# Optimization experiments

Hardware: AMD Instinct MI355X
Metric: run time of the kernel (lower is better)

## Reference

```python
import jax, jax.numpy as jnp
import numpy as np
from jax import lax

# --- COSMO-SAC constants (defaults from the layer) ---
T = 623.15
Q0 = 79.53
R0 = 66.69
C_HB = 85580.0
RGAS = 8.3144598 / 4184.0
SIG_HB = 0.0084
EPS = 3.667
AEFF = 7.5
EO = 0.0002395
ZC = 10.0
X0 = 0.235
X1 = 1.0 - 0.235
N_SIGMA = 51
N_ITERS = 50


def _deltaw():
    s = np.linspace(-0.025, 0.025, N_SIGMA)
    sigma_m = np.tile(s, (N_SIGMA, 1))          # rows of grid values
    sigma_n = sigma_m.T
    sigma_acc = np.tril(sigma_n) + np.triu(sigma_m, 1)
    sigma_don = np.tril(sigma_m) + np.triu(sigma_n, 1)
    fpol = (EPS - 1.0) / (EPS + 0.5)
    alpha = 0.3 * AEFF ** 1.5 / EO
    alpha_prime = fpol * alpha
    dw = (alpha_prime / 2.0 * (sigma_m + sigma_n) ** 2
          + C_HB * np.maximum(0.0, sigma_acc - SIG_HB) * np.minimum(0.0, sigma_don + SIG_HB))
    return jnp.asarray(dw, jnp.float32)

DELTAW = _deltaw()                       # [51,51]
SSS = jnp.exp(-DELTAW / (RGAS * T))      # [51,51]


def get_Gamma(psigma):
    """50-step fixed-point solve. psigma: [B,51] -> Gamma: [B,51]."""
    AA = SSS[None, :, :] * psigma[:, None, :]   # [B,51,51]
    def step(G, _):
        Gnew = 1.0 / jnp.einsum('bmn,bn->bm', AA, G)
        return (Gnew + G) * 0.5, None
    G, _ = lax.scan(step, jnp.ones_like(psigma), None, length=N_ITERS)
    return G


def setup_inputs() -> dict:
    key = jax.random.key(0)
    k1, k2, k3, k4 = jax.random.split(key, 4)
    B = 32768
    return {
        "input_my_sigma": jax.random.uniform(k1, (B, N_SIGMA), dtype=jnp.float32),
        "v_compound": jax.random.uniform(k2, (B,), dtype=jnp.float32),
        "input_vt_sigma": jax.random.uniform(k3, (B, N_SIGMA, 2), dtype=jnp.float32),
        "v_vt": jax.random.uniform(k4, (B,), dtype=jnp.float32),
    }


def reference(input_my_sigma, v_compound, input_vt_sigma, v_vt):
    my = input_my_sigma                 # [B,51]
    vt = input_vt_sigma[:, :, 1]        # [B,51]
    A0 = jnp.sum(my, axis=1)            # [B]
    A1 = jnp.sum(vt, axis=1)            # [B]

    psigma_mix = (X0 * my + X1 * vt) / (X0 * A0[:, None] + X1 * A1[:, None])
    lnGamma_mix = jnp.log(get_Gamma(psigma_mix))       # [B,51]

    # residual part for component i = 0
    psigma = my / A0[:, None]
    lnGammai = jnp.log(get_Gamma(psigma))              # [B,51]
    lng_resid = A0 / AEFF * jnp.sum(psigma * (lnGamma_mix - lnGammai), axis=1)

    # combinatorial part (Staverman-Guggenheim)
    q0 = A0 / Q0
    q1 = A1 / Q0
    r0 = v_compound / R0
    r1 = v_vt / R0
    xq = X0 * q0 + X1 * q1
    xr = X0 * r0 + X1 * r1
    theta = X0 * q0 / xq
    phi = X0 * r0 / xr
    l0 = ZC / 2.0 * (r0 - q0) - (r0 - 1.0)
    l1 = ZC / 2.0 * (r1 - q1) - (r1 - 1.0)
    xl = X0 * l0 + X1 * l1
    lng_comb = (jnp.log(phi / X0) + ZC / 2.0 * q0 * jnp.log(theta / phi)
                + l0 - phi / X0 * xl)

    return (lng_resid + lng_comb)[:, None]             # [B,1]
```

## Files before the change

### kernel.cpp

```cpp
#include <hip/hip_runtime.h>

typedef __bf16 bf16;
typedef __attribute__((ext_vector_type(8))) bf16 bf16x8;
typedef __attribute__((ext_vector_type(4))) float f32x4;

namespace {

constexpr int NITERS = 50;
constexpr int KEXACT = 16;

constexpr double csqrt(double x) {
  double s = x > 1 ? x : 1;
  for (int i = 0; i < 60; ++i) s = 0.5 * (s + x / s);
  return s;
}
constexpr double AP_D =
    ((3.667 - 1.0) / (3.667 + 0.5)) * (0.3 * (7.5 * csqrt(7.5)) / 0.0002395);
constexpr double RGAST_D = (8.3144598 / 4184.0) * 623.15;

__device__ __forceinline__ float sss_val(int i, int j) {
  if (i > 50 || j > 50) return 0.0f;
  const float si = -0.025f + 0.001f * (float)i;
  const float sj = -0.025f + 0.001f * (float)j;
  const float acc = fmaxf(0.0f, fmaxf(si, sj) - 0.0084f);
  const float don = fminf(0.0f, fminf(si, sj) + 0.0084f);
  const float dw = (float)(AP_D * 0.5) * (si + sj) * (si + sj) + 85580.0f * acc * don;
  return expf(-dw * (float)(1.0 / RGAST_D));
}

__device__ __forceinline__ int slot2row(int slot) {
  if (slot < 48) return slot;
  if ((slot & 3) == 0 && slot < 60) return 48 + ((slot - 48) >> 2);
  return 99;
}

__device__ __forceinline__ float fast_log(float x) {
  return __builtin_amdgcn_logf(x) * 0.69314718056f;
}

__device__ __forceinline__ f32x4 mfma(bf16x8 a, bf16x8 b, f32x4 c) {
  return __builtin_amdgcn_mfma_f32_16x16x32_bf16(a, b, c, 0, 0, 0);
}

__device__ __forceinline__ unsigned cvt_pk(float lo, float hi) {
  unsigned r;
  asm("v_cvt_pk_bf16_f32 %0, %1, %2" : "=v"(r) : "v"(lo), "v"(hi));
  return r;
}

union B8 { unsigned u[4]; bf16x8 v; };

}

__global__ __launch_bounds__(256, 4) void cosmo_mfma_r8(
    const float* __restrict__ my_sigma,
    const float* __restrict__ v_comp,
    const float* __restrict__ vt_sigma,
    const float* __restrict__ v_vt,
    float* __restrict__ out,
    int B)
{
  const int lane = threadIdx.x & 63;
  const int wv   = threadIdx.x >> 6;
  const int s    = lane & 15;
  const int g    = lane >> 4;
  const int task = s & 1;
  const int e    = blockIdx.x * 32 + wv * 8 + (s >> 1);
  const bool ein = (e < B);
  const int  ec  = ein ? e : 0;

  float A0, A1;
  float wh[13], Gt[13], rc[13];
  {
    float myv[13], vtv[13];
#pragma unroll
    for (int t = 0; t < 4; ++t)
#pragma unroll
      for (int r = 0; r < 4; ++r) {
        const int li = 4 * t + r;
        if (li >= 13) continue;
        const int n  = slot2row(16 * t + 4 * g + r);
        const bool nv = (n < 51) && ein;
        const int nc = (n < 51) ? n : 50;
        myv[li] = nv ? my_sigma[(size_t)ec * 51 + nc] : 0.0f;
        vtv[li] = nv ? vt_sigma[((size_t)ec * 51 + nc) * 2 + 1] : 0.0f;
      }
    float pA0 = 0.f, pA1 = 0.f;
#pragma unroll
    for (int i = 0; i < 13; ++i) { pA0 += myv[i]; pA1 += vtv[i]; }
    pA0 += __shfl_xor(pA0, 16, 64); pA0 += __shfl_xor(pA0, 32, 64);
    pA1 += __shfl_xor(pA1, 16, 64); pA1 += __shfl_xor(pA1, 32, 64);
    A0 = pA0; A1 = pA1;

    const float den  = task ? (0.235f * pA0 + 0.765f * pA1) : pA0;
    const float rden = __builtin_amdgcn_rcpf(den);
    const float rdh  = 0.5f * rden;
#pragma unroll
    for (int i = 0; i < 13; ++i) {
      const float num = task ? (0.235f * myv[i] + 0.765f * vtv[i]) : myv[i];
      Gt[i] = num * rden;
      wh[i] = num * rdh;
      rc[i] = 1.0f;
    }
  }

  bf16x8 afr[4][2];
#pragma unroll
  for (int tp = 0; tp < 4; ++tp)
#pragma unroll
    for (int kt = 0; kt < 2; ++kt) {
      bf16x8 v;
#pragma unroll
      for (int i = 0; i < 8; ++i) {
        const int kslot = 16 * (2 * kt + (i >> 2)) + 4 * g + (i & 3);
        v[i] = (bf16)sss_val(slot2row(16 * tp + s), slot2row(kslot));
      }
      afr[tp][kt] = v;
    }

  f32x4 pad3;
  pad3[0] = (g == 3) ? 1.0f : 0.0f;
  pad3[1] = pad3[2] = pad3[3] = 1.0f;

  f32x4 acc[4];

  auto matvec = [&]() {
    B8 x0, x1;
    x0.u[0] = cvt_pk(Gt[0],  Gt[1]);
    x0.u[1] = cvt_pk(Gt[2],  Gt[3]);
    x0.u[2] = cvt_pk(Gt[4],  Gt[5]);
    x0.u[3] = cvt_pk(Gt[6],  Gt[7]);
    x1.u[0] = cvt_pk(Gt[8],  Gt[9]);
    x1.u[1] = cvt_pk(Gt[10], Gt[11]);
    x1.u[2] = cvt_pk(Gt[12], 0.0f);
    x1.u[3] = 0;
    const bf16x8 b0 = x0.v, b1 = x1.v;

    const f32x4 z = {};
#pragma unroll
    for (int tp = 0; tp < 3; ++tp) acc[tp] = mfma(afr[tp][0], b0, z);
    acc[3] = mfma(afr[3][0], b0, pad3);
#pragma unroll
    for (int tp = 0; tp < 4; ++tp) acc[tp] = mfma(afr[tp][1], b1, acc[tp]);
  };

  auto upd_rcp = [&]() {
#pragma unroll
    for (int tp = 0; tp < 3; ++tp)
#pragma unroll
      for (int r = 0; r < 4; ++r) {
        const int i = 4 * tp + r;
        const float rcv = __builtin_amdgcn_rcpf(acc[tp][r]);
        rc[i] = rcv;
        Gt[i] = __builtin_fmaf(wh[i], rcv, 0.5f * Gt[i]);
      }
    {
      const float rcv = __builtin_amdgcn_rcpf(acc[3][0]);
      rc[12] = rcv;
      Gt[12] = __builtin_fmaf(wh[12], rcv, 0.5f * Gt[12]);
    }
  };

  auto upd_newton = [&]() {
#pragma unroll
    for (int tp = 0; tp < 3; ++tp)
#pragma unroll
      for (int r = 0; r < 4; ++r) {
        const int i = 4 * tp + r;
        const float nr  = __builtin_fmaf(-acc[tp][r], rc[i], 2.0f);
        const float rcv = rc[i] * nr;
        rc[i] = rcv;
        Gt[i] = __builtin_fmaf(wh[i], rcv, 0.5f * Gt[i]);
      }
    {
      const float nr  = __builtin_fmaf(-acc[3][0], rc[12], 2.0f);
      const float rcv = rc[12] * nr;
      rc[12] = rcv;
      Gt[12] = __builtin_fmaf(wh[12], rcv, 0.5f * Gt[12]);
    }
  };

  matvec();
#pragma unroll
  for (int it = 0; it < KEXACT; ++it) { upd_rcp(); matvec(); }
#pragma unroll
  for (int it = KEXACT; it < NITERS - 1; ++it) { upd_newton(); matvec(); }
  upd_newton();

  const float rA0 = __builtin_amdgcn_rcpf(A0);
  float Sp = 0.f;
#pragma unroll
  for (int t = 0; t < 4; ++t)
#pragma unroll
    for (int r = 0; r < 4; ++r) {
      const int li = 4 * t + r;
      if (li >= 13) continue;
      const int n = slot2row(16 * t + 4 * g + r);
      if (n < 51) {
        const float p  = (ein ? my_sigma[(size_t)ec * 51 + n] : 0.0f) * rA0;
        const float gg = (wh[li] != 0.0f)
                           ? Gt[li] * (0.5f * __builtin_amdgcn_rcpf(wh[li])) : 1.0f;
        Sp += p * __builtin_amdgcn_logf(gg);
      }
    }
  Sp += __shfl_xor(Sp, 16, 64);
  Sp += __shfl_xor(Sp, 32, 64);
  const float St = Sp * 0.69314718056f;
  const float So = __shfl_xor(St, 1, 64);

  if (task == 0 && g == 0 && ein) {
    const float lng_resid = A0 * (1.0f / 7.5f) * (So - St);
    const float v0  = v_comp[e];
    const float v1v = v_vt[e];
    const float q0 = A0 * (1.0f / 79.53f), q1 = A1 * (1.0f / 79.53f);
    const float r0 = v0 * (1.0f / 66.69f), r1 = v1v * (1.0f / 66.69f);
    const float xq = 0.235f * q0 + 0.765f * q1;
    const float xr = 0.235f * r0 + 0.765f * r1;
    const float theta = 0.235f * q0 * __builtin_amdgcn_rcpf(xq);
    const float phi   = 0.235f * r0 * __builtin_amdgcn_rcpf(xr);
    const float l0 = 5.0f * (r0 - q0) - (r0 - 1.0f);
    const float l1 = 5.0f * (r1 - q1) - (r1 - 1.0f);
    const float xl = 0.235f * l0 + 0.765f * l1;
    const float lng_comb = fast_log(phi * (1.0f / 0.235f))
                         + 5.0f * q0 * fast_log(theta * __builtin_amdgcn_rcpf(phi))
                         + l0 - (phi * (1.0f / 0.235f)) * xl;
    out[e] = lng_resid + lng_comb;
  }
}

extern "C" void kernel_launch(void* const* d_in, const int* in_sizes, int n_in,
                              void* d_out, int out_size, void* d_ws, size_t ws_size,
                              hipStream_t stream) {
  const float* my  = (const float*)d_in[0];
  const float* vc  = (const float*)d_in[1];
  const float* vts = (const float*)d_in[2];
  const float* vvt = (const float*)d_in[3];
  float* out = (float*)d_out;
  const int B = in_sizes[1];
  const int grid = (B + 31) / 32;
  cosmo_mfma_r8<<<grid, 256, 0, stream>>>(my, vc, vts, vvt, out, B);
}
```

Baseline: 109.6 us.

## Switch fixed-point matvec to 32x32x16 MFMA with 16 systems per wave

Replaces the 16x16x32 MFMA tiling with 32x32x16 bf16 MFMAs. Each wave now handles 32 right-hand sides (16 elements × 2 tasks) against a 64-row padded SSS matrix, so the compact slot remapping is no longer needed. This doubles the elements per block and halves the grid. The iteration loops are no longer unrolled and the occupancy hint drops to 2, trading more registers per lane for fewer MFMA issues per element. It also pads to 64 rows instead of the tighter 51-row packing, so some of the extra work is wasted.

```diff
diff --git a/kernel.cpp b/kernel.cpp
--- a/kernel.cpp
+++ b/kernel.cpp
@@ -2,7 +2,7 @@
 
 typedef __bf16 bf16;
 typedef __attribute__((ext_vector_type(8))) bf16 bf16x8;
-typedef __attribute__((ext_vector_type(4))) float f32x4;
+typedef __attribute__((ext_vector_type(16))) float f32x16;
 
 namespace {
 
@@ -28,18 +28,12 @@
   return expf(-dw * (float)(1.0 / RGAST_D));
 }
 
-__device__ __forceinline__ int slot2row(int slot) {
-  if (slot < 48) return slot;
-  if ((slot & 3) == 0 && slot < 60) return 48 + ((slot - 48) >> 2);
-  return 99;
-}
-
 __device__ __forceinline__ float fast_log(float x) {
   return __builtin_amdgcn_logf(x) * 0.69314718056f;
 }
 
-__device__ __forceinline__ f32x4 mfma(bf16x8 a, bf16x8 b, f32x4 c) {
-  return __builtin_amdgcn_mfma_f32_16x16x32_bf16(a, b, c, 0, 0, 0);
+__device__ __forceinline__ f32x16 mfma32(bf16x8 a, bf16x8 b, f32x16 c) {
+  return __builtin_amdgcn_mfma_f32_32x32x16_bf16(a, b, c, 0, 0, 0);
 }
 
 __device__ __forceinline__ unsigned cvt_pk(float lo, float hi) {
@@ -50,9 +44,17 @@
 
 union B8 { unsigned u[4]; bf16x8 v; };
 
-}
-
-__global__ __launch_bounds__(256, 4) void cosmo_mfma_r8(
+__device__ __forceinline__ constexpr int slot_of(int t, int reg, int h) {
+  return 32 * t + (reg & 3) + 8 * (reg >> 2) + 4 * h;
+}
+
+__device__ __forceinline__ constexpr bool live_class(int t, int reg) {
+  return (t == 0) || (reg < 11);
+}
+
+}
+
+__global__ __launch_bounds__(256, 2) void cosmo_mfma_r9(
     const float* __restrict__ my_sigma,
     const float* __restrict__ v_comp,
     const float* __restrict__ vt_sigma,
@@ -62,153 +64,147 @@
 {
   const int lane = threadIdx.x & 63;
   const int wv   = threadIdx.x >> 6;
-  const int s    = lane & 15;
-  const int g    = lane >> 4;
-  const int task = s & 1;
-  const int e    = blockIdx.x * 32 + wv * 8 + (s >> 1);
+  const int n    = lane & 31;
+  const int h    = lane >> 5;
+  const int task = n & 1;
+  const int e    = blockIdx.x * 64 + wv * 16 + (n >> 1);
   const bool ein = (e < B);
   const int  ec  = ein ? e : 0;
 
+  float Gt[2][16], wh[2][16], rc[2][16];
+#pragma unroll
+  for (int t = 0; t < 2; ++t)
+#pragma unroll
+    for (int r = 0; r < 16; ++r) { Gt[t][r] = 0.0f; wh[t][r] = 0.0f; rc[t][r] = 1.0f; }
+
   float A0, A1;
-  float wh[13], Gt[13], rc[13];
   {
-    float myv[13], vtv[13];
-#pragma unroll
-    for (int t = 0; t < 4; ++t)
-#pragma unroll
-      for (int r = 0; r < 4; ++r) {
-        const int li = 4 * t + r;
-        if (li >= 13) continue;
-        const int n  = slot2row(16 * t + 4 * g + r);
-        const bool nv = (n < 51) && ein;
-        const int nc = (n < 51) ? n : 50;
-        myv[li] = nv ? my_sigma[(size_t)ec * 51 + nc] : 0.0f;
-        vtv[li] = nv ? vt_sigma[((size_t)ec * 51 + nc) * 2 + 1] : 0.0f;
-      }
+    float myv[2][16], vtv[2][16];
     float pA0 = 0.f, pA1 = 0.f;
 #pragma unroll
-    for (int i = 0; i < 13; ++i) { pA0 += myv[i]; pA1 += vtv[i]; }
-    pA0 += __shfl_xor(pA0, 16, 64); pA0 += __shfl_xor(pA0, 32, 64);
-    pA1 += __shfl_xor(pA1, 16, 64); pA1 += __shfl_xor(pA1, 32, 64);
+    for (int t = 0; t < 2; ++t)
+#pragma unroll
+      for (int r = 0; r < 16; ++r) {
+        if (!live_class(t, r)) continue;
+        const int slot = slot_of(t, r, h);
+        const bool nv = (slot < 51) && ein;
+        const int sc = (slot < 51) ? slot : 50;
+        myv[t][r] = nv ? my_sigma[(size_t)ec * 51 + sc] : 0.0f;
+        vtv[t][r] = nv ? vt_sigma[((size_t)ec * 51 + sc) * 2 + 1] : 0.0f;
+        pA0 += myv[t][r]; pA1 += vtv[t][r];
+      }
+    pA0 += __shfl_xor(pA0, 32, 64);
+    pA1 += __shfl_xor(pA1, 32, 64);
     A0 = pA0; A1 = pA1;
 
     const float den  = task ? (0.235f * pA0 + 0.765f * pA1) : pA0;
     const float rden = __builtin_amdgcn_rcpf(den);
     const float rdh  = 0.5f * rden;
 #pragma unroll
-    for (int i = 0; i < 13; ++i) {
-      const float num = task ? (0.235f * myv[i] + 0.765f * vtv[i]) : myv[i];
-      Gt[i] = num * rden;
-      wh[i] = num * rdh;
-      rc[i] = 1.0f;
-    }
+    for (int t = 0; t < 2; ++t)
+#pragma unroll
+      for (int r = 0; r < 16; ++r) {
+        if (!live_class(t, r)) continue;
+        const float num = task ? (0.235f * myv[t][r] + 0.765f * vtv[t][r]) : myv[t][r];
+        Gt[t][r] = num * rden;
+        wh[t][r] = num * rdh;
+      }
   }
 
-  bf16x8 afr[4][2];
-#pragma unroll
-  for (int tp = 0; tp < 4; ++tp)
-#pragma unroll
-    for (int kt = 0; kt < 2; ++kt) {
+  bf16x8 afr[2][4];
+#pragma unroll
+  for (int t = 0; t < 2; ++t)
+#pragma unroll
+    for (int c = 0; c < 4; ++c) {
       bf16x8 v;
 #pragma unroll
-      for (int i = 0; i < 8; ++i) {
-        const int kslot = 16 * (2 * kt + (i >> 2)) + 4 * g + (i & 3);
-        v[i] = (bf16)sss_val(slot2row(16 * tp + s), slot2row(kslot));
-      }
-      afr[tp][kt] = v;
-    }
-
-  f32x4 pad3;
-  pad3[0] = (g == 3) ? 1.0f : 0.0f;
-  pad3[1] = pad3[2] = pad3[3] = 1.0f;
-
-  f32x4 acc[4];
+      for (int j = 0; j < 8; ++j) {
+        const int kslot = 32 * (c >> 1) + 16 * (c & 1) + 8 * (j >> 2) + (j & 3) + 4 * h;
+        v[j] = (bf16)sss_val(32 * t + n, kslot);
+      }
+      afr[t][c] = v;
+    }
+
+  f32x16 pinit[2];
+#pragma unroll
+  for (int t = 0; t < 2; ++t)
+#pragma unroll
+    for (int r = 0; r < 16; ++r)
+      pinit[t][r] = (slot_of(t, r, h) >= 51) ? 1.0f : 0.0f;
+
+  f32x16 acc[2];
 
   auto matvec = [&]() {
-    B8 x0, x1;
-    x0.u[0] = cvt_pk(Gt[0],  Gt[1]);
-    x0.u[1] = cvt_pk(Gt[2],  Gt[3]);
-    x0.u[2] = cvt_pk(Gt[4],  Gt[5]);
-    x0.u[3] = cvt_pk(Gt[6],  Gt[7]);
-    x1.u[0] = cvt_pk(Gt[8],  Gt[9]);
-    x1.u[1] = cvt_pk(Gt[10], Gt[11]);
-    x1.u[2] = cvt_pk(Gt[12], 0.0f);
-    x1.u[3] = 0;
-    const bf16x8 b0 = x0.v, b1 = x1.v;
-
-    const f32x4 z = {};
-#pragma unroll
-    for (int tp = 0; tp < 3; ++tp) acc[tp] = mfma(afr[tp][0], b0, z);
-    acc[3] = mfma(afr[3][0], b0, pad3);
-#pragma unroll
-    for (int tp = 0; tp < 4; ++tp) acc[tp] = mfma(afr[tp][1], b1, acc[tp]);
+    B8 b[4];
+#pragma unroll
+    for (int c = 0; c < 4; ++c) {
+      const int t = c >> 1, rb = 8 * (c & 1);
+      b[c].u[0] = cvt_pk(Gt[t][rb + 0], Gt[t][rb + 1]);
+      b[c].u[1] = cvt_pk(Gt[t][rb + 2], Gt[t][rb + 3]);
+      b[c].u[2] = cvt_pk(Gt[t][rb + 4], Gt[t][rb + 5]);
+      b[c].u[3] = cvt_pk(Gt[t][rb + 6], Gt[t][rb + 7]);
+    }
+    acc[0] = mfma32(afr[0][0], b[0].v, pinit[0]);
+    acc[1] = mfma32(afr[1][0], b[0].v, pinit[1]);
+#pragma unroll
+    for (int c = 1; c < 4; ++c) {
+      acc[0] = mfma32(afr[0][c], b[c].v, acc[0]);
+      acc[1] = mfma32(afr[1][c], b[c].v, acc[1]);
+    }
   };
 
   auto upd_rcp = [&]() {
 #pragma unroll
-    for (int tp = 0; tp < 3; ++tp)
-#pragma unroll
-      for (int r = 0; r < 4; ++r) {
-        const int i = 4 * tp + r;
-        const float rcv = __builtin_amdgcn_rcpf(acc[tp][r]);
-        rc[i] = rcv;
-        Gt[i] = __builtin_fmaf(wh[i], rcv, 0.5f * Gt[i]);
-      }
-    {
-      const float rcv = __builtin_amdgcn_rcpf(acc[3][0]);
-      rc[12] = rcv;
-      Gt[12] = __builtin_fmaf(wh[12], rcv, 0.5f * Gt[12]);
-    }
+    for (int t = 0; t < 2; ++t)
+#pragma unroll
+      for (int r = 0; r < 16; ++r) {
+        if (!live_class(t, r)) continue;
+        const float rcv = __builtin_amdgcn_rcpf(acc[t][r]);
+        rc[t][r] = rcv;
+        Gt[t][r] = __builtin_fmaf(wh[t][r], rcv, 0.5f * Gt[t][r]);
+      }
   };
 
   auto upd_newton = [&]() {
 #pragma unroll
-    for (int tp = 0; tp < 3; ++tp)
-#pragma unroll
-      for (int r = 0; r < 4; ++r) {
-        const int i = 4 * tp + r;
-        const float nr  = __builtin_fmaf(-acc[tp][r], rc[i], 2.0f);
-        const float rcv = rc[i] * nr;
-        rc[i] = rcv;
-        Gt[i] = __builtin_fmaf(wh[i], rcv, 0.5f * Gt[i]);
-      }
-    {
-      const float nr  = __builtin_fmaf(-acc[3][0], rc[12], 2.0f);
-      const float rcv = rc[12] * nr;
-      rc[12] = rcv;
-      Gt[12] = __builtin_fmaf(wh[12], rcv, 0.5f * Gt[12]);
-    }
+    for (int t = 0; t < 2; ++t)
+#pragma unroll
+      for (int r = 0; r < 16; ++r) {
+        if (!live_class(t, r)) continue;
+        const float nr  = __builtin_fmaf(-acc[t][r], rc[t][r], 2.0f);
+        const float rcv = rc[t][r] * nr;
+        rc[t][r] = rcv;
+        Gt[t][r] = __builtin_fmaf(wh[t][r], rcv, 0.5f * Gt[t][r]);
+      }
   };
 
   matvec();
-#pragma unroll
+#pragma unroll 1
   for (int it = 0; it < KEXACT; ++it) { upd_rcp(); matvec(); }
-#pragma unroll
+#pragma unroll 1
   for (int it = KEXACT; it < NITERS - 1; ++it) { upd_newton(); matvec(); }
   upd_newton();
 
   const float rA0 = __builtin_amdgcn_rcpf(A0);
   float Sp = 0.f;
 #pragma unroll
-  for (int t = 0; t < 4; ++t)
-#pragma unroll
-    for (int r = 0; r < 4; ++r) {
-      const int li = 4 * t + r;
-      if (li >= 13) continue;
-      const int n = slot2row(16 * t + 4 * g + r);
-      if (n < 51) {
-        const float p  = (ein ? my_sigma[(size_t)ec * 51 + n] : 0.0f) * rA0;
-        const float gg = (wh[li] != 0.0f)
-                           ? Gt[li] * (0.5f * __builtin_amdgcn_rcpf(wh[li])) : 1.0f;
-        Sp += p * __builtin_amdgcn_logf(gg);
-      }
-    }
-  Sp += __shfl_xor(Sp, 16, 64);
+  for (int t = 0; t < 2; ++t)
+#pragma unroll
+    for (int r = 0; r < 16; ++r) {
+      if (!live_class(t, r)) continue;
+      const int slot = slot_of(t, r, h);
+      const bool nv = (slot < 51) && ein;
+      const int sc = (slot < 51) ? slot : 50;
+      const float p  = (nv ? my_sigma[(size_t)ec * 51 + sc] : 0.0f) * rA0;
+      const float gg = (wh[t][r] != 0.0f)
+                         ? Gt[t][r] * (0.5f * __builtin_amdgcn_rcpf(wh[t][r])) : 1.0f;
+      Sp += p * __builtin_amdgcn_logf(gg);
+    }
   Sp += __shfl_xor(Sp, 32, 64);
   const float St = Sp * 0.69314718056f;
   const float So = __shfl_xor(St, 1, 64);
 
-  if (task == 0 && g == 0 && ein) {
+  if (task == 0 && h == 0 && ein) {
     const float lng_resid = A0 * (1.0f / 7.5f) * (So - St);
     const float v0  = v_comp[e];
     const float v1v = v_vt[e];
@@ -237,6 +233,6 @@
   const float* vvt = (const float*)d_in[3];
   float* out = (float*)d_out;
   const int B = in_sizes[1];
-  const int grid = (B + 31) / 32;
-  cosmo_mfma_r8<<<grid, 256, 0, stream>>>(my, vc, vts, vvt, out, B);
-}
+  const int grid = (B + 63) / 64;
+  cosmo_mfma_r9<<<grid, 256, 0, stream>>>(my, vc, vts, vvt, out, B);
+}
```

After: 108.5 us. About the same (-1.1%).
